# Kernel optimization log

Measured on AMD Instinct MI355X. Metric: run time of the kernel, lower is better.

## Reference

```python
import jax, jax.numpy as jnp
import numpy as np

DIM = 180
HEADS = 6
HEAD_DIM = DIM // HEADS
SCALE = HEAD_DIM ** (-0.5)
BW, N, K = 8192, 64, 16


def setup_inputs() -> dict:
    key = jax.random.key(0)
    ks = jax.random.split(key, 6)
    return {
        "x": jax.random.normal(ks[0], (BW, N, DIM), dtype=jnp.float32),
        "bpe_windows": jax.random.normal(ks[1], (BW, N, K), dtype=jnp.float32),
        "qkv_w": jax.random.normal(ks[2], (3 * DIM, DIM), dtype=jnp.float32) * 0.05,
        "qkv_b": jax.random.normal(ks[3], (3 * DIM,), dtype=jnp.float32) * 0.05,
        "proj_w": jax.random.normal(ks[4], (DIM, DIM), dtype=jnp.float32) * 0.05,
        "proj_b": jax.random.normal(ks[5], (DIM,), dtype=jnp.float32) * 0.05,
        "tau": jnp.ones((HEADS, 1, 1), dtype=jnp.float32),
    }


def reference(x, bpe_windows, qkv_w, qkv_b, proj_w, proj_b, tau):
    B_, n, C = x.shape
    # qkv projection -> (3, B_, H, N, hd)
    qkv = (x @ qkv_w.T + qkv_b).reshape(B_, n, 3, HEADS, HEAD_DIM)
    qkv = jnp.transpose(qkv, (2, 0, 3, 1, 4))
    q, k, v = qkv[0], qkv[1], qkv[2]
    q = q * SCALE
    attn = jnp.einsum("bhid,bhjd->bhij", q, k)  # (B_, H, N, N)
    # geodesic bias from BPE embeddings: d_B(i,j) = ||bpe_i - bpe_j||_2
    diff = bpe_windows[:, :, None, :] - bpe_windows[:, None, :, :]  # (B_, N, N, K)
    d_B = jnp.sqrt(jnp.sum(diff * diff, axis=-1))  # (B_, N, N)
    log_W_geo = -d_B[:, None, :, :] / jnp.clip(tau, 1e-6)[None]  # (B_, H, N, N)
    attn = jax.nn.softmax(attn + log_W_geo, axis=-1)
    out = jnp.einsum("bhij,bhjd->bhid", attn, v)  # (B_, H, N, hd)
    out = jnp.transpose(out, (0, 2, 1, 3)).reshape(B_, n, C)
    return out @ proj_w.T + proj_b
```

## Files before the change

### kernel.cpp

```cpp
#include <hip/hip_runtime.h>
#include <math.h>

typedef __attribute__((ext_vector_type(8))) short short8b;
typedef __attribute__((ext_vector_type(4))) float f32x4;

#define NWIN 8192
#define NT   512
#define SCALE 0.18257418583505536f

#define XB_P 200
#define QK_P 40
#define VT_P 72
#define DB_P 65
#define S_P  65
#define PP_P 72
#define OST_P 180

#define OFF_XB  0
#define OFF_Q   25600
#define OFF_K   56320
#define OFF_VT  87040
#define OFF_DB  114688
#define OFF_S   131328
#define OFF_P   147968
#define LDS_BYTES 157184
#define OFF_OST OFF_Q

#define WQ_ROWS 544
#define WK 192

__device__ __forceinline__ unsigned short f2bf(float f) {
    union { float f; unsigned int u; } v; v.f = f;
    unsigned int r = (v.u + 0x7FFFu + ((v.u >> 16) & 1u)) >> 16;
    return (unsigned short)r;
}

__global__ void prep_weights(const float* __restrict__ qkv_w,
                             const float* __restrict__ proj_w,
                             unsigned short* __restrict__ wq,
                             unsigned short* __restrict__ wp)
{
    const int i = blockIdx.x * 256 + threadIdx.x;
    if (i < WQ_ROWS * WK) {
        const int r = i / WK, c = i % WK;
        const float v = (r < 540 && c < 180) ? qkv_w[r * 180 + c] : 0.f;
        wq[i] = f2bf(v);
    }
    const int j = i - WQ_ROWS * WK;
    if (j >= 0 && j < 192 * WK) {
        const int r = j / WK, c = j % WK;
        const float v = (r < 180 && c < 180) ? proj_w[r * 180 + c] : 0.f;
        wp[j] = f2bf(v);
    }
}

__global__ void __launch_bounds__(NT, 1)
waga_mfma(const float* __restrict__ x,
          const float* __restrict__ bpe,
          const unsigned short* __restrict__ wq,
          const unsigned short* __restrict__ wp,
          const float* __restrict__ qkv_b,
          const float* __restrict__ proj_b,
          const float* __restrict__ tau,
          float* __restrict__ out)
{
    extern __shared__ char smem[];
    unsigned short* xb    = (unsigned short*)(smem + OFF_XB);
    unsigned short* q_lds = (unsigned short*)(smem + OFF_Q);
    unsigned short* k_lds = (unsigned short*)(smem + OFF_K);
    unsigned short* vT    = (unsigned short*)(smem + OFF_VT);
    float*          dBs   = (float*)(smem + OFF_DB);
    float*          S_lds = (float*)(smem + OFF_S);
    float*          bpes  = (float*)(smem + OFF_S);
    unsigned short* P_lds = (unsigned short*)(smem + OFF_P);
    float*          ostage= (float*)(smem + OFF_OST);
    unsigned short* att   = xb;

    const int b = blockIdx.x;
    const int t = threadIdx.x;
    const int w = t >> 6;
    const int l = t & 63;
    const int lr = l & 15;
    const int g  = l >> 4;

    {
        f32x4 z = {0.f, 0.f, 0.f, 0.f};
        f32x4* p = (f32x4*)smem;
        for (int i = t; i < LDS_BYTES / 16; i += NT) p[i] = z;
    }
    __syncthreads();

    {
        const float* xw = x + (size_t)b * (64 * 180);
        for (int i = t; i < 64 * 45; i += NT) {
            const int n = i / 45, c4 = i % 45;
            const float4 v = *reinterpret_cast<const float4*>(xw + i * 4);
            unsigned short* d = xb + n * XB_P + c4 * 4;
            d[0] = f2bf(v.x); d[1] = f2bf(v.y); d[2] = f2bf(v.z); d[3] = f2bf(v.w);
        }
        const float* bw = bpe + (size_t)b * (64 * 16);
        for (int i = t; i < 64 * 4; i += NT) {
            const int n = i / 4, k4 = i % 4;
            const float4 v = *reinterpret_cast<const float4*>(bw + i * 4);
            float* d = bpes + n * 20 + 4 * k4;
            d[0] = v.x; d[1] = v.y; d[2] = v.z; d[3] = v.w;
        }
    }
    __syncthreads();

    {
        const int ti = t >> 4, tj = t & 15;
        float acc[2][4] = {{0.f,0.f,0.f,0.f},{0.f,0.f,0.f,0.f}};
        #pragma unroll
        for (int k4 = 0; k4 < 4; ++k4) {
            const float4 a0 = *reinterpret_cast<const float4*>(bpes + ti * 20 + 4 * k4);
            const float4 a1 = *reinterpret_cast<const float4*>(bpes + (ti + 32) * 20 + 4 * k4);
            #pragma unroll
            for (int e = 0; e < 4; ++e) {
                const float4 bb = *reinterpret_cast<const float4*>(bpes + (tj + 16 * e) * 20 + 4 * k4);
                float d;
                d = a0.x - bb.x; acc[0][e] += d * d;
                d = a0.y - bb.y; acc[0][e] += d * d;
                d = a0.z - bb.z; acc[0][e] += d * d;
                d = a0.w - bb.w; acc[0][e] += d * d;
                d = a1.x - bb.x; acc[1][e] += d * d;
                d = a1.y - bb.y; acc[1][e] += d * d;
                d = a1.z - bb.z; acc[1][e] += d * d;
                d = a1.w - bb.w; acc[1][e] += d * d;
            }
        }
        #pragma unroll
        for (int r = 0; r < 2; ++r)
            #pragma unroll
            for (int e = 0; e < 4; ++e)
                dBs[(ti + 32 * r) * DB_P + tj + 16 * e] = sqrtf(acc[r][e]);
    }

    {
        const int ntbase = 4 * w;
        f32x4 acc[4][4];
        #pragma unroll
        for (int q = 0; q < 4; ++q) {
            const int m = (ntbase + q) * 16 + lr;
            const float bias = (m < 540) ? qkv_b[m] : 0.f;
            #pragma unroll
            for (int mt = 0; mt < 4; ++mt) {
                acc[q][mt][0] = bias; acc[q][mt][1] = bias;
                acc[q][mt][2] = bias; acc[q][mt][3] = bias;
            }
        }
        for (int kk = 0; kk < 6; ++kk) {
            short8b bfr[4];
            #pragma unroll
            for (int q = 0; q < 4; ++q)
                bfr[q] = *reinterpret_cast<const short8b*>(wq + ((ntbase + q) * 16 + lr) * WK + kk * 32 + g * 8);
            #pragma unroll
            for (int mt = 0; mt < 4; ++mt) {
                const short8b af = *reinterpret_cast<const short8b*>(xb + (mt * 16 + lr) * XB_P + kk * 32 + g * 8);
                #pragma unroll
                for (int q = 0; q < 4; ++q)
                    acc[q][mt] = __builtin_amdgcn_mfma_f32_16x16x32_bf16(af, bfr[q], acc[q][mt], 0, 0, 0);
            }
        }
        #pragma unroll
        for (int q = 0; q < 4; ++q) {
            const int m = (ntbase + q) * 16 + lr;
            if (m < 540) {
                const int which = m / 180, mm = m % 180, hh = mm / 30, dd = mm % 30;
                unsigned short* dst; int ts; float sc;
                if (which == 0)      { dst = q_lds + hh * 2560 + dd;      ts = QK_P; sc = SCALE; }
                else if (which == 1) { dst = k_lds + hh * 2560 + dd;      ts = QK_P; sc = 1.f; }
                else                 { dst = vT + hh * 2304 + dd * VT_P;  ts = 1;    sc = 1.f; }
                #pragma unroll
                for (int mt = 0; mt < 4; ++mt)
                    #pragma unroll
                    for (int i = 0; i < 4; ++i) {
                        const int tok = mt * 16 + g * 4 + i;
                        dst[tok * ts] = f2bf(acc[q][mt][i] * sc);
                    }
            }
        }
        if (w >= 6) {
            const int nt = 26 + w;
            const int m = nt * 16 + lr;
            f32x4 acc2[4];
            const float bias = (m < 540) ? qkv_b[m] : 0.f;
            #pragma unroll
            for (int mt = 0; mt < 4; ++mt) {
                acc2[mt][0] = bias; acc2[mt][1] = bias; acc2[mt][2] = bias; acc2[mt][3] = bias;
            }
            for (int kk = 0; kk < 6; ++kk) {
                const short8b bf = *reinterpret_cast<const short8b*>(wq + m * WK + kk * 32 + g * 8);
                #pragma unroll
                for (int mt = 0; mt < 4; ++mt) {
                    const short8b af = *reinterpret_cast<const short8b*>(xb + (mt * 16 + lr) * XB_P + kk * 32 + g * 8);
                    acc2[mt] = __builtin_amdgcn_mfma_f32_16x16x32_bf16(af, bf, acc2[mt], 0, 0, 0);
                }
            }
            if (m < 540) {
                const int which = m / 180, mm = m % 180, hh = mm / 30, dd = mm % 30;
                unsigned short* dst; int ts; float sc;
                if (which == 0)      { dst = q_lds + hh * 2560 + dd;      ts = QK_P; sc = SCALE; }
                else if (which == 1) { dst = k_lds + hh * 2560 + dd;      ts = QK_P; sc = 1.f; }
                else                 { dst = vT + hh * 2304 + dd * VT_P;  ts = 1;    sc = 1.f; }
                #pragma unroll
                for (int mt = 0; mt < 4; ++mt)
                    #pragma unroll
                    for (int i = 0; i < 4; ++i) {
                        const int tok = mt * 16 + g * 4 + i;
                        dst[tok * ts] = f2bf(acc2[mt][i] * sc);
                    }
            }
        }
    }
    __syncthreads();

    for (int h = 0; h < 6; ++h) {
        const float it = 1.f / fmaxf(tau[h], 1e-6f);
        for (int tid = w; tid < 16; tid += 8) {
            const int mt = tid >> 2, nt2 = tid & 3;
            f32x4 acc;
            #pragma unroll
            for (int i = 0; i < 4; ++i)
                acc[i] = -dBs[(mt * 16 + g * 4 + i) * DB_P + nt2 * 16 + lr] * it;
            const short8b af = *reinterpret_cast<const short8b*>(q_lds + h * 2560 + (mt * 16 + lr) * QK_P + g * 8);
            const short8b bf = *reinterpret_cast<const short8b*>(k_lds + h * 2560 + (nt2 * 16 + lr) * QK_P + g * 8);
            acc = __builtin_amdgcn_mfma_f32_16x16x32_bf16(af, bf, acc, 0, 0, 0);
            #pragma unroll
            for (int i = 0; i < 4; ++i)
                S_lds[(mt * 16 + g * 4 + i) * S_P + nt2 * 16 + lr] = acc[i];
        }
        __syncthreads();

        {
            const int tn = t >> 4, tj = t & 15;
            #pragma unroll
            for (int r = 0; r < 2; ++r) {
                const int row = tn + 32 * r;
                float s0 = S_lds[row * S_P + tj];
                float s1 = S_lds[row * S_P + tj + 16];
                float s2 = S_lds[row * S_P + tj + 32];
                float s3 = S_lds[row * S_P + tj + 48];
                float mx = fmaxf(fmaxf(s0, s1), fmaxf(s2, s3));
                #pragma unroll
                for (int o = 1; o < 16; o <<= 1) mx = fmaxf(mx, __shfl_xor(mx, o, 16));
                float p0 = __expf(s0 - mx), p1 = __expf(s1 - mx);
                float p2 = __expf(s2 - mx), p3 = __expf(s3 - mx);
                float sum = p0 + p1 + p2 + p3;
                #pragma unroll
                for (int o = 1; o < 16; o <<= 1) sum += __shfl_xor(sum, o, 16);
                const float inv = 1.f / sum;
                P_lds[row * PP_P + tj]      = f2bf(p0 * inv);
                P_lds[row * PP_P + tj + 16] = f2bf(p1 * inv);
                P_lds[row * PP_P + tj + 32] = f2bf(p2 * inv);
                P_lds[row * PP_P + tj + 48] = f2bf(p3 * inv);
            }
        }
        __syncthreads();

        {
            const int mt = w >> 1, nt2 = w & 1;
            f32x4 acc = {0.f, 0.f, 0.f, 0.f};
            #pragma unroll
            for (int ks = 0; ks < 2; ++ks) {
                const short8b af = *reinterpret_cast<const short8b*>(P_lds + (mt * 16 + lr) * PP_P + ks * 32 + g * 8);
                const short8b bf = *reinterpret_cast<const short8b*>(vT + h * 2304 + (nt2 * 16 + lr) * VT_P + ks * 32 + g * 8);
                acc = __builtin_amdgcn_mfma_f32_16x16x32_bf16(af, bf, acc, 0, 0, 0);
            }
            const int dd = nt2 * 16 + lr;
            if (dd < 30) {
                #pragma unroll
                for (int i = 0; i < 4; ++i)
                    att[(mt * 16 + g * 4 + i) * XB_P + h * 30 + dd] = f2bf(acc[i]);
            }
        }
        __syncthreads();
    }

    {
        for (int nt = w; nt < 12; nt += 8) {
            f32x4 acc[4];
            #pragma unroll
            for (int mt = 0; mt < 4; ++mt) { acc[mt][0]=0.f; acc[mt][1]=0.f; acc[mt][2]=0.f; acc[mt][3]=0.f; }
            for (int kk = 0; kk < 6; ++kk) {
                const short8b bf = *reinterpret_cast<const short8b*>(wp + (nt * 16 + lr) * WK + kk * 32 + g * 8);
                #pragma unroll
                for (int mt = 0; mt < 4; ++mt) {
                    const short8b af = *reinterpret_cast<const short8b*>(att + (mt * 16 + lr) * XB_P + kk * 32 + g * 8);
                    acc[mt] = __builtin_amdgcn_mfma_f32_16x16x32_bf16(af, bf, acc[mt], 0, 0, 0);
                }
            }
            const int mcol = nt * 16 + lr;
            if (mcol < 180) {
                const float pb = proj_b[mcol];
                #pragma unroll
                for (int mt = 0; mt < 4; ++mt)
                    #pragma unroll
                    for (int i = 0; i < 4; ++i)
                        ostage[(mt * 16 + g * 4 + i) * OST_P + mcol] = acc[mt][i] + pb;
            }
        }
    }
    __syncthreads();

    {
        float4* src = (float4*)ostage;
        float4* dst = (float4*)(out + (size_t)b * (64 * 180));
        for (int i = t; i < 64 * 180 / 4; i += NT) dst[i] = src[i];
    }
}

extern "C" void kernel_launch(void* const* d_in, const int* in_sizes, int n_in,
                              void* d_out, int out_size, void* d_ws, size_t ws_size,
                              hipStream_t stream) {
    (void)in_sizes; (void)n_in; (void)out_size; (void)ws_size;
    const float* x      = (const float*)d_in[0];
    const float* bpe    = (const float*)d_in[1];
    const float* qkv_w  = (const float*)d_in[2];
    const float* qkv_b  = (const float*)d_in[3];
    const float* proj_w = (const float*)d_in[4];
    const float* proj_b = (const float*)d_in[5];
    const float* tau    = (const float*)d_in[6];

    unsigned short* wq = (unsigned short*)d_ws;
    unsigned short* wp = wq + WQ_ROWS * WK;

    prep_weights<<<(WQ_ROWS * WK + 192 * WK + 255) / 256, 256, 0, stream>>>(qkv_w, proj_w, wq, wp);

    (void)hipFuncSetAttribute((const void*)waga_mfma,
                              hipFuncAttributeMaxDynamicSharedMemorySize,
                              LDS_BYTES);
    waga_mfma<<<NWIN, NT, LDS_BYTES, stream>>>(x, bpe, wq, wp, qkv_b, proj_b, tau,
                                               (float*)d_out);
}
```

Measured before the change: 841.9 us.

## Double block size and fuse per-head attention into per-wave tiles

Raises the block to 1024 threads (16 waves) and redistributes the QKV GEMM, distance computation and output projection across them. The per-head attention loop with three block-wide barriers per head is replaced by independent per-wave (head, row-tile) units that compute scores, softmax in registers and P·V using a private LDS scratch, which removes most of the __syncthreads. It also interleaves Q and K in one LDS buffer, zeroes only the padding instead of all of LDS, and vectorizes the LDS stores. Costs: register pressure is higher under 1024-thread bounds, and only 24 attention units exist for 16 waves, so the work is unevenly split.

```diff
diff --git a/kernel.cpp b/kernel.cpp
--- a/kernel.cpp
+++ b/kernel.cpp
@@ -3,36 +3,35 @@
 
 typedef __attribute__((ext_vector_type(8))) short short8b;
 typedef __attribute__((ext_vector_type(4))) float f32x4;
+typedef __attribute__((ext_vector_type(4))) unsigned short ushort4b;
+typedef __attribute__((ext_vector_type(2))) unsigned short ushort2b;
 
 #define NWIN 8192
-#define NT   512
+#define NT   1024
 #define SCALE 0.18257418583505536f
 
-#define XB_P 200
-#define QK_P 40
-#define VT_P 72
-#define DB_P 65
-#define S_P  65
-#define PP_P 72
+#define XB_P  200
+#define QK_P  392
+#define VT_P  72
+#define DB_P  66
+#define SCR_P 80
 #define OST_P 180
 
 #define OFF_XB  0
-#define OFF_Q   25600
-#define OFF_K   56320
-#define OFF_VT  87040
-#define OFF_DB  114688
-#define OFF_S   131328
-#define OFF_P   147968
-#define LDS_BYTES 157184
-#define OFF_OST OFF_Q
+#define OFF_QK  25600
+#define OFF_VT  75776
+#define OFF_DB  103424
+#define OFF_SCR 120320
+#define LDS_BYTES 161280
+#define OFF_OST OFF_QK
+#define OFF_BPE OFF_SCR
 
 #define WQ_ROWS 544
 #define WK 192
 
 __device__ __forceinline__ unsigned short f2bf(float f) {
     union { float f; unsigned int u; } v; v.f = f;
-    unsigned int r = (v.u + 0x7FFFu + ((v.u >> 16) & 1u)) >> 16;
-    return (unsigned short)r;
+    return (unsigned short)((v.u + 0x7FFFu + ((v.u >> 16) & 1u)) >> 16);
 }
 
 __global__ void prep_weights(const float* __restrict__ qkv_w,
@@ -43,18 +42,16 @@
     const int i = blockIdx.x * 256 + threadIdx.x;
     if (i < WQ_ROWS * WK) {
         const int r = i / WK, c = i % WK;
-        const float v = (r < 540 && c < 180) ? qkv_w[r * 180 + c] : 0.f;
-        wq[i] = f2bf(v);
+        wq[i] = f2bf((r < 540 && c < 180) ? qkv_w[r * 180 + c] : 0.f);
     }
     const int j = i - WQ_ROWS * WK;
     if (j >= 0 && j < 192 * WK) {
         const int r = j / WK, c = j % WK;
-        const float v = (r < 180 && c < 180) ? proj_w[r * 180 + c] : 0.f;
-        wp[j] = f2bf(v);
+        wp[j] = f2bf((r < 180 && c < 180) ? proj_w[r * 180 + c] : 0.f);
     }
 }
 
-__global__ void __launch_bounds__(NT, 1)
+__global__ void __launch_bounds__(NT, 4)
 waga_mfma(const float* __restrict__ x,
           const float* __restrict__ bpe,
           const unsigned short* __restrict__ wq,
@@ -65,16 +62,14 @@
           float* __restrict__ out)
 {
     extern __shared__ char smem[];
-    unsigned short* xb    = (unsigned short*)(smem + OFF_XB);
-    unsigned short* q_lds = (unsigned short*)(smem + OFF_Q);
-    unsigned short* k_lds = (unsigned short*)(smem + OFF_K);
-    unsigned short* vT    = (unsigned short*)(smem + OFF_VT);
-    float*          dBs   = (float*)(smem + OFF_DB);
-    float*          S_lds = (float*)(smem + OFF_S);
-    float*          bpes  = (float*)(smem + OFF_S);
-    unsigned short* P_lds = (unsigned short*)(smem + OFF_P);
-    float*          ostage= (float*)(smem + OFF_OST);
-    unsigned short* att   = xb;
+    unsigned short* xb   = (unsigned short*)(smem + OFF_XB);
+    unsigned short* qk   = (unsigned short*)(smem + OFF_QK);
+    unsigned short* vT   = (unsigned short*)(smem + OFF_VT);
+    float*          dBs  = (float*)(smem + OFF_DB);
+    unsigned short* scr  = (unsigned short*)(smem + OFF_SCR);
+    float*          bpes = (float*)(smem + OFF_BPE);
+    unsigned short* att  = xb;
+    float*          ostage = (float*)(smem + OFF_OST);
 
     const int b = blockIdx.x;
     const int t = threadIdx.x;
@@ -83,228 +78,199 @@
     const int lr = l & 15;
     const int g  = l >> 4;
 
-    {
-        f32x4 z = {0.f, 0.f, 0.f, 0.f};
-        f32x4* p = (f32x4*)smem;
-        for (int i = t; i < LDS_BYTES / 16; i += NT) p[i] = z;
-    }
-    __syncthreads();
-
+    if (t < 320) {
+        const int n = t / 5, c = t % 5;
+        ushort4b z = {0, 0, 0, 0};
+        *reinterpret_cast<ushort4b*>(xb + n * XB_P + 180 + 4 * c) = z;
+    }
+    if (t < 768) {
+        const int tok = t / 12, r = t % 12;
+        const int col = (r >> 1) * 64 + (r & 1) * 32 + 30;
+        ushort2b z2 = {0, 0};
+        *reinterpret_cast<ushort2b*>(qk + tok * QK_P + col) = z2;
+    }
     {
         const float* xw = x + (size_t)b * (64 * 180);
         for (int i = t; i < 64 * 45; i += NT) {
             const int n = i / 45, c4 = i % 45;
             const float4 v = *reinterpret_cast<const float4*>(xw + i * 4);
-            unsigned short* d = xb + n * XB_P + c4 * 4;
-            d[0] = f2bf(v.x); d[1] = f2bf(v.y); d[2] = f2bf(v.z); d[3] = f2bf(v.w);
-        }
+            ushort4b o;
+            o[0] = f2bf(v.x); o[1] = f2bf(v.y); o[2] = f2bf(v.z); o[3] = f2bf(v.w);
+            *reinterpret_cast<ushort4b*>(xb + n * XB_P + c4 * 4) = o;
+        }
+    }
+    if (t < 256) {
         const float* bw = bpe + (size_t)b * (64 * 16);
-        for (int i = t; i < 64 * 4; i += NT) {
-            const int n = i / 4, k4 = i % 4;
-            const float4 v = *reinterpret_cast<const float4*>(bw + i * 4);
-            float* d = bpes + n * 20 + 4 * k4;
-            d[0] = v.x; d[1] = v.y; d[2] = v.z; d[3] = v.w;
-        }
+        const int n = t >> 2, k4 = t & 3;
+        const float4 v = *reinterpret_cast<const float4*>(bw + t * 4);
+        *reinterpret_cast<float4*>(bpes + n * 20 + 4 * k4) = v;
     }
     __syncthreads();
 
     {
         const int ti = t >> 4, tj = t & 15;
-        float acc[2][4] = {{0.f,0.f,0.f,0.f},{0.f,0.f,0.f,0.f}};
+        float acc[4] = {0.f, 0.f, 0.f, 0.f};
         #pragma unroll
         for (int k4 = 0; k4 < 4; ++k4) {
-            const float4 a0 = *reinterpret_cast<const float4*>(bpes + ti * 20 + 4 * k4);
-            const float4 a1 = *reinterpret_cast<const float4*>(bpes + (ti + 32) * 20 + 4 * k4);
+            const float4 a = *reinterpret_cast<const float4*>(bpes + ti * 20 + 4 * k4);
             #pragma unroll
             for (int e = 0; e < 4; ++e) {
                 const float4 bb = *reinterpret_cast<const float4*>(bpes + (tj + 16 * e) * 20 + 4 * k4);
                 float d;
-                d = a0.x - bb.x; acc[0][e] += d * d;
-                d = a0.y - bb.y; acc[0][e] += d * d;
-                d = a0.z - bb.z; acc[0][e] += d * d;
-                d = a0.w - bb.w; acc[0][e] += d * d;
-                d = a1.x - bb.x; acc[1][e] += d * d;
-                d = a1.y - bb.y; acc[1][e] += d * d;
-                d = a1.z - bb.z; acc[1][e] += d * d;
-                d = a1.w - bb.w; acc[1][e] += d * d;
+                d = a.x - bb.x; acc[e] += d * d;
+                d = a.y - bb.y; acc[e] += d * d;
+                d = a.z - bb.z; acc[e] += d * d;
+                d = a.w - bb.w; acc[e] += d * d;
             }
         }
         #pragma unroll
-        for (int r = 0; r < 2; ++r)
-            #pragma unroll
-            for (int e = 0; e < 4; ++e)
-                dBs[(ti + 32 * r) * DB_P + tj + 16 * e] = sqrtf(acc[r][e]);
-    }
-
-    {
-        const int ntbase = 4 * w;
-        f32x4 acc[4][4];
+        for (int e = 0; e < 4; ++e)
+            dBs[ti * DB_P + tj + 16 * e] = sqrtf(acc[e]);
+    }
+
+    {
+        const int nt0 = w, nt1 = w + 16, nt2q = 32 + w;
+        const bool has2 = (w < 2);
+        const int m0 = nt0 * 16 + lr, m1 = nt1 * 16 + lr, m2 = nt2q * 16 + lr;
+        f32x4 acc0[4], acc1[4], acc2[4];
+        const float b0 = (m0 < 540) ? qkv_b[m0] : 0.f;
+        const float b1 = (m1 < 540) ? qkv_b[m1] : 0.f;
+        const float b2 = (has2 && m2 < 540) ? qkv_b[m2] : 0.f;
         #pragma unroll
-        for (int q = 0; q < 4; ++q) {
-            const int m = (ntbase + q) * 16 + lr;
-            const float bias = (m < 540) ? qkv_b[m] : 0.f;
-            #pragma unroll
-            for (int mt = 0; mt < 4; ++mt) {
-                acc[q][mt][0] = bias; acc[q][mt][1] = bias;
-                acc[q][mt][2] = bias; acc[q][mt][3] = bias;
-            }
+        for (int mt = 0; mt < 4; ++mt) {
+            #pragma unroll
+            for (int i = 0; i < 4; ++i) { acc0[mt][i] = b0; acc1[mt][i] = b1; acc2[mt][i] = b2; }
         }
         for (int kk = 0; kk < 6; ++kk) {
-            short8b bfr[4];
-            #pragma unroll
-            for (int q = 0; q < 4; ++q)
-                bfr[q] = *reinterpret_cast<const short8b*>(wq + ((ntbase + q) * 16 + lr) * WK + kk * 32 + g * 8);
-            #pragma unroll
-            for (int mt = 0; mt < 4; ++mt) {
-                const short8b af = *reinterpret_cast<const short8b*>(xb + (mt * 16 + lr) * XB_P + kk * 32 + g * 8);
-                #pragma unroll
-                for (int q = 0; q < 4; ++q)
-                    acc[q][mt] = __builtin_amdgcn_mfma_f32_16x16x32_bf16(af, bfr[q], acc[q][mt], 0, 0, 0);
-            }
-        }
-        #pragma unroll
-        for (int q = 0; q < 4; ++q) {
-            const int m = (ntbase + q) * 16 + lr;
+            short8b af[4];
+            #pragma unroll
+            for (int mt = 0; mt < 4; ++mt)
+                af[mt] = *reinterpret_cast<const short8b*>(xb + (mt * 16 + lr) * XB_P + kk * 32 + g * 8);
+            const short8b bf0 = *reinterpret_cast<const short8b*>(wq + (size_t)m0 * WK + kk * 32 + g * 8);
+            #pragma unroll
+            for (int mt = 0; mt < 4; ++mt)
+                acc0[mt] = __builtin_amdgcn_mfma_f32_16x16x32_bf16(af[mt], bf0, acc0[mt], 0, 0, 0);
+            const short8b bf1 = *reinterpret_cast<const short8b*>(wq + (size_t)m1 * WK + kk * 32 + g * 8);
+            #pragma unroll
+            for (int mt = 0; mt < 4; ++mt)
+                acc1[mt] = __builtin_amdgcn_mfma_f32_16x16x32_bf16(af[mt], bf1, acc1[mt], 0, 0, 0);
+            if (has2) {
+                const short8b bf2 = *reinterpret_cast<const short8b*>(wq + (size_t)m2 * WK + kk * 32 + g * 8);
+                #pragma unroll
+                for (int mt = 0; mt < 4; ++mt)
+                    acc2[mt] = __builtin_amdgcn_mfma_f32_16x16x32_bf16(af[mt], bf2, acc2[mt], 0, 0, 0);
+            }
+        }
+        auto epi = [&](int m, f32x4* acc) {
             if (m < 540) {
                 const int which = m / 180, mm = m % 180, hh = mm / 30, dd = mm % 30;
-                unsigned short* dst; int ts; float sc;
-                if (which == 0)      { dst = q_lds + hh * 2560 + dd;      ts = QK_P; sc = SCALE; }
-                else if (which == 1) { dst = k_lds + hh * 2560 + dd;      ts = QK_P; sc = 1.f; }
-                else                 { dst = vT + hh * 2304 + dd * VT_P;  ts = 1;    sc = 1.f; }
                 #pragma unroll
                 for (int mt = 0; mt < 4; ++mt)
                     #pragma unroll
                     for (int i = 0; i < 4; ++i) {
                         const int tok = mt * 16 + g * 4 + i;
-                        dst[tok * ts] = f2bf(acc[q][mt][i] * sc);
+                        const float v = acc[mt][i];
+                        if (which == 0)      qk[tok * QK_P + hh * 64 + dd] = f2bf(v * SCALE);
+                        else if (which == 1) qk[tok * QK_P + hh * 64 + 32 + dd] = f2bf(v);
+                        else                 vT[hh * 2304 + dd * VT_P + tok] = f2bf(v);
                     }
             }
-        }
-        if (w >= 6) {
-            const int nt = 26 + w;
-            const int m = nt * 16 + lr;
-            f32x4 acc2[4];
-            const float bias = (m < 540) ? qkv_b[m] : 0.f;
-            #pragma unroll
-            for (int mt = 0; mt < 4; ++mt) {
-                acc2[mt][0] = bias; acc2[mt][1] = bias; acc2[mt][2] = bias; acc2[mt][3] = bias;
-            }
+        };
+        epi(m0, acc0);
+        epi(m1, acc1);
+        if (has2) epi(m2, acc2);
+    }
+    __syncthreads();
+
+    {
+        unsigned short* myscr = scr + w * (16 * SCR_P);
+        for (int u = w; u < 24; u += 16) {
+            const int h = u >> 2, mt = u & 3;
+            const float it = 1.f / fmaxf(tau[h], 1e-6f);
+            f32x4 s[4];
+            #pragma unroll
+            for (int nt2 = 0; nt2 < 4; ++nt2)
+                #pragma unroll
+                for (int i = 0; i < 4; ++i)
+                    s[nt2][i] = -dBs[(mt * 16 + g * 4 + i) * DB_P + nt2 * 16 + lr] * it;
+            const short8b qa = *reinterpret_cast<const short8b*>(qk + (mt * 16 + lr) * QK_P + h * 64 + g * 8);
+            #pragma unroll
+            for (int nt2 = 0; nt2 < 4; ++nt2) {
+                const short8b kb = *reinterpret_cast<const short8b*>(qk + (nt2 * 16 + lr) * QK_P + h * 64 + 32 + g * 8);
+                s[nt2] = __builtin_amdgcn_mfma_f32_16x16x32_bf16(qa, kb, s[nt2], 0, 0, 0);
+            }
+            float mx[4], sm[4];
+            #pragma unroll
+            for (int i = 0; i < 4; ++i)
+                mx[i] = fmaxf(fmaxf(s[0][i], s[1][i]), fmaxf(s[2][i], s[3][i]));
+            #pragma unroll
+            for (int o = 1; o < 16; o <<= 1)
+                #pragma unroll
+                for (int i = 0; i < 4; ++i)
+                    mx[i] = fmaxf(mx[i], __shfl_xor(mx[i], o, 16));
+            #pragma unroll
+            for (int i = 0; i < 4; ++i) sm[i] = 0.f;
+            #pragma unroll
+            for (int nt2 = 0; nt2 < 4; ++nt2)
+                #pragma unroll
+                for (int i = 0; i < 4; ++i) {
+                    const float p = __expf(s[nt2][i] - mx[i]);
+                    s[nt2][i] = p; sm[i] += p;
+                }
+            #pragma unroll
+            for (int o = 1; o < 16; o <<= 1)
+                #pragma unroll
+                for (int i = 0; i < 4; ++i)
+                    sm[i] += __shfl_xor(sm[i], o, 16);
+            #pragma unroll
+            for (int i = 0; i < 4; ++i) sm[i] = 1.f / sm[i];
+            #pragma unroll
+            for (int nt2 = 0; nt2 < 4; ++nt2)
+                #pragma unroll
+                for (int i = 0; i < 4; ++i)
+                    myscr[(g * 4 + i) * SCR_P + nt2 * 16 + lr] = f2bf(s[nt2][i] * sm[i]);
+            f32x4 o0 = {0.f, 0.f, 0.f, 0.f}, o1 = {0.f, 0.f, 0.f, 0.f};
+            #pragma unroll
+            for (int ks = 0; ks < 2; ++ks) {
+                const short8b pa = *reinterpret_cast<const short8b*>(myscr + lr * SCR_P + ks * 32 + g * 8);
+                const short8b v0 = *reinterpret_cast<const short8b*>(vT + h * 2304 + lr * VT_P + ks * 32 + g * 8);
+                const short8b v1 = *reinterpret_cast<const short8b*>(vT + h * 2304 + (16 + lr) * VT_P + ks * 32 + g * 8);
+                o0 = __builtin_amdgcn_mfma_f32_16x16x32_bf16(pa, v0, o0, 0, 0, 0);
+                o1 = __builtin_amdgcn_mfma_f32_16x16x32_bf16(pa, v1, o1, 0, 0, 0);
+            }
+            #pragma unroll
+            for (int i = 0; i < 4; ++i) {
+                const int tok = mt * 16 + g * 4 + i;
+                att[tok * XB_P + h * 30 + lr] = f2bf(o0[i]);
+                if (lr < 14)
+                    att[tok * XB_P + h * 30 + 16 + lr] = f2bf(o1[i]);
+            }
+        }
+    }
+    __syncthreads();
+
+    {
+        for (int tid = 3 * w; tid < 3 * w + 3; ++tid) {
+            const int nt = tid >> 2, mt = tid & 3;
+            f32x4 acc = {0.f, 0.f, 0.f, 0.f};
             for (int kk = 0; kk < 6; ++kk) {
-                const short8b bf = *reinterpret_cast<const short8b*>(wq + m * WK + kk * 32 + g * 8);
-                #pragma unroll
-                for (int mt = 0; mt < 4; ++mt) {
-                    const short8b af = *reinterpret_cast<const short8b*>(xb + (mt * 16 + lr) * XB_P + kk * 32 + g * 8);
-                    acc2[mt] = __builtin_amdgcn_mfma_f32_16x16x32_bf16(af, bf, acc2[mt], 0, 0, 0);
-                }
-            }
-            if (m < 540) {
-                const int which = m / 180, mm = m % 180, hh = mm / 30, dd = mm % 30;
-                unsigned short* dst; int ts; float sc;
-                if (which == 0)      { dst = q_lds + hh * 2560 + dd;      ts = QK_P; sc = SCALE; }
-                else if (which == 1) { dst = k_lds + hh * 2560 + dd;      ts = QK_P; sc = 1.f; }
-                else                 { dst = vT + hh * 2304 + dd * VT_P;  ts = 1;    sc = 1.f; }
-                #pragma unroll
-                for (int mt = 0; mt < 4; ++mt)
-                    #pragma unroll
-                    for (int i = 0; i < 4; ++i) {
-                        const int tok = mt * 16 + g * 4 + i;
-                        dst[tok * ts] = f2bf(acc2[mt][i] * sc);
-                    }
-            }
-        }
-    }
-    __syncthreads();
-
-    for (int h = 0; h < 6; ++h) {
-        const float it = 1.f / fmaxf(tau[h], 1e-6f);
-        for (int tid = w; tid < 16; tid += 8) {
-            const int mt = tid >> 2, nt2 = tid & 3;
-            f32x4 acc;
-            #pragma unroll
-            for (int i = 0; i < 4; ++i)
-                acc[i] = -dBs[(mt * 16 + g * 4 + i) * DB_P + nt2 * 16 + lr] * it;
-            const short8b af = *reinterpret_cast<const short8b*>(q_lds + h * 2560 + (mt * 16 + lr) * QK_P + g * 8);
-            const short8b bf = *reinterpret_cast<const short8b*>(k_lds + h * 2560 + (nt2 * 16 + lr) * QK_P + g * 8);
-            acc = __builtin_amdgcn_mfma_f32_16x16x32_bf16(af, bf, acc, 0, 0, 0);
-            #pragma unroll
-            for (int i = 0; i < 4; ++i)
-                S_lds[(mt * 16 + g * 4 + i) * S_P + nt2 * 16 + lr] = acc[i];
-        }
-        __syncthreads();
-
-        {
-            const int tn = t >> 4, tj = t & 15;
-            #pragma unroll
-            for (int r = 0; r < 2; ++r) {
-                const int row = tn + 32 * r;
-                float s0 = S_lds[row * S_P + tj];
-                float s1 = S_lds[row * S_P + tj + 16];
-                float s2 = S_lds[row * S_P + tj + 32];
-                float s3 = S_lds[row * S_P + tj + 48];
-                float mx = fmaxf(fmaxf(s0, s1), fmaxf(s2, s3));
-                #pragma unroll
-                for (int o = 1; o < 16; o <<= 1) mx = fmaxf(mx, __shfl_xor(mx, o, 16));
-                float p0 = __expf(s0 - mx), p1 = __expf(s1 - mx);
-                float p2 = __expf(s2 - mx), p3 = __expf(s3 - mx);
-                float sum = p0 + p1 + p2 + p3;
-                #pragma unroll
-                for (int o = 1; o < 16; o <<= 1) sum += __shfl_xor(sum, o, 16);
-                const float inv = 1.f / sum;
-                P_lds[row * PP_P + tj]      = f2bf(p0 * inv);
-                P_lds[row * PP_P + tj + 16] = f2bf(p1 * inv);
-                P_lds[row * PP_P + tj + 32] = f2bf(p2 * inv);
-                P_lds[row * PP_P + tj + 48] = f2bf(p3 * inv);
-            }
-        }
-        __syncthreads();
-
-        {
-            const int mt = w >> 1, nt2 = w & 1;
-            f32x4 acc = {0.f, 0.f, 0.f, 0.f};
-            #pragma unroll
-            for (int ks = 0; ks < 2; ++ks) {
-                const short8b af = *reinterpret_cast<const short8b*>(P_lds + (mt * 16 + lr) * PP_P + ks * 32 + g * 8);
-                const short8b bf = *reinterpret_cast<const short8b*>(vT + h * 2304 + (nt2 * 16 + lr) * VT_P + ks * 32 + g * 8);
+                const short8b af = *reinterpret_cast<const short8b*>(att + (mt * 16 + lr) * XB_P + kk * 32 + g * 8);
+                const short8b bf = *reinterpret_cast<const short8b*>(wp + (nt * 16 + lr) * WK + kk * 32 + g * 8);
                 acc = __builtin_amdgcn_mfma_f32_16x16x32_bf16(af, bf, acc, 0, 0, 0);
-            }
-            const int dd = nt2 * 16 + lr;
-            if (dd < 30) {
-                #pragma unroll
-                for (int i = 0; i < 4; ++i)
-                    att[(mt * 16 + g * 4 + i) * XB_P + h * 30 + dd] = f2bf(acc[i]);
-            }
-        }
-        __syncthreads();
-    }
-
-    {
-        for (int nt = w; nt < 12; nt += 8) {
-            f32x4 acc[4];
-            #pragma unroll
-            for (int mt = 0; mt < 4; ++mt) { acc[mt][0]=0.f; acc[mt][1]=0.f; acc[mt][2]=0.f; acc[mt][3]=0.f; }
-            for (int kk = 0; kk < 6; ++kk) {
-                const short8b bf = *reinterpret_cast<const short8b*>(wp + (nt * 16 + lr) * WK + kk * 32 + g * 8);
-                #pragma unroll
-                for (int mt = 0; mt < 4; ++mt) {
-                    const short8b af = *reinterpret_cast<const short8b*>(att + (mt * 16 + lr) * XB_P + kk * 32 + g * 8);
-                    acc[mt] = __builtin_amdgcn_mfma_f32_16x16x32_bf16(af, bf, acc[mt], 0, 0, 0);
-                }
             }
             const int mcol = nt * 16 + lr;
             if (mcol < 180) {
                 const float pb = proj_b[mcol];
                 #pragma unroll
-                for (int mt = 0; mt < 4; ++mt)
-                    #pragma unroll
-                    for (int i = 0; i < 4; ++i)
-                        ostage[(mt * 16 + g * 4 + i) * OST_P + mcol] = acc[mt][i] + pb;
+                for (int i = 0; i < 4; ++i)
+                    ostage[(mt * 16 + g * 4 + i) * OST_P + mcol] = acc[i] + pb;
             }
         }
     }
     __syncthreads();
 
     {
-        float4* src = (float4*)ostage;
+        const float4* src = (const float4*)ostage;
         float4* dst = (float4*)(out + (size_t)b * (64 * 180));
         for (int i = t; i < 64 * 180 / 4; i += NT) dst[i] = src[i];
     }
```

Measured after the change: 775.5 us. 1.09x faster.
